# Kernel optimization log

Hardware: AMD Instinct MI355X
Metric: run time of the kernel (lower is better)

Reference implementation:

```python
import jax, jax.numpy as jnp
import numpy as np

B, A, NB = 8, 1024, 64          # batch, atoms, neighbors
NAB, NF, NG, NI = 128, 128, 25, 3  # atom basis, filters, gaussians, interactions
CUT = 5.0
MAXZ = 100
LOG2 = float(np.log(2.0))

def ssp(x):
    # shifted softplus: log(0.5) + softplus(x)
    return jax.nn.softplus(x) - LOG2

def setup_inputs() -> dict:
    key = jax.random.key(0)
    ks = jax.random.split(key, 12)
    positions = jax.random.uniform(ks[0], (B, A, 3), jnp.float32, 0.0, 10.0)
    cell = jnp.zeros((B, 3, 3), jnp.float32)
    cell_offset = jnp.zeros((B, A, NB, 3), jnp.float32)
    # self-avoiding neighbor indices in [0, A)
    off = jax.random.randint(ks[1], (B, A, NB), 1, A)
    neighbors = ((jnp.arange(A)[None, :, None] + off) % A).astype(jnp.int32)
    neighbor_mask = jnp.ones((B, A, NB), jnp.float32)
    atom_mask = jnp.ones((B, A), jnp.float32)
    atomic_numbers = jax.random.randint(ks[2], (B, A), 1, MAXZ).astype(jnp.int32)
    s = 0.05
    emb = (jax.random.normal(ks[3], (MAXZ, NAB)) * 0.1).at[0].set(0.0)  # padding_idx=0
    fw1 = jax.random.normal(ks[4], (NI, NG, NF)) * s
    fb1 = jnp.zeros((NI, NF), jnp.float32)
    fw2 = jax.random.normal(ks[5], (NI, NF, NF)) * s
    fb2 = jnp.zeros((NI, NF), jnp.float32)
    in2f_w = jax.random.normal(ks[6], (NI, NAB, NF)) * s
    f2out_w = jax.random.normal(ks[7], (NI, NF, NAB)) * s
    f2out_b = jnp.zeros((NI, NAB), jnp.float32)
    dense_w = jax.random.normal(ks[8], (NI, NAB, NAB)) * s
    dense_b = jnp.zeros((NI, NAB), jnp.float32)
    return dict(positions=positions, cell=cell, cell_offset=cell_offset,
                neighbor_mask=neighbor_mask, atom_mask=atom_mask,
                emb=emb, fw1=fw1, fb1=fb1, fw2=fw2, fb2=fb2,
                in2f_w=in2f_w, f2out_w=f2out_w, f2out_b=f2out_b,
                dense_w=dense_w, dense_b=dense_b,
                atomic_numbers=atomic_numbers, neighbors=neighbors)

def reference(positions, cell, cell_offset, neighbor_mask, atom_mask,
              emb, fw1, fb1, fw2, fb2, in2f_w, f2out_w, f2out_b,
              dense_w, dense_b, atomic_numbers, neighbors):
    x = emb[atomic_numbers]                                   # (B,A,NAB)
    nb = neighbors.reshape(B, A * NB)
    # atom distances with PBC offsets
    pos_j = jnp.take_along_axis(positions, nb[..., None], axis=1).reshape(B, A, NB, 3)
    pos_j = pos_j + jnp.einsum('banc,bcd->band', cell_offset, cell)
    dvec = pos_j - positions[:, :, None, :]
    d2 = jnp.sum(dvec * dvec, axis=-1)                        # (B,A,NB)
    r_ij = jnp.sqrt(jnp.where(neighbor_mask > 0, d2, 1.0)) * neighbor_mask
    # gaussian smearing of distances
    offsets = jnp.linspace(0.0, CUT, NG, dtype=jnp.float32)
    width = offsets[1] - offsets[0]
    coeff = -0.5 / (width * width)
    f_ij = jnp.exp(coeff * (r_ij[..., None] - offsets) ** 2)  # (B,A,NB,NG)
    # cosine cutoff
    C = 0.5 * (jnp.cos(r_ij * jnp.pi / CUT) + 1.0) * (r_ij < CUT)
    for i in range(NI):
        # filter-generating network
        W = ssp(f_ij @ fw1[i] + fb1[i]) @ fw2[i] + fb2[i]     # (B,A,NB,NF)
        W = W * C[..., None]
        # CFConv: project, gather neighbors, modulate, scatter-sum
        y = x @ in2f_w[i]                                     # (B,A,NF)
        y_nbh = jnp.take_along_axis(y, nb[..., None], axis=1).reshape(B, A, NB, NF)
        agg = jnp.sum(y_nbh * W * neighbor_mask[..., None], axis=2)  # (B,A,NF)
        v = ssp(agg @ f2out_w[i] + f2out_b[i])                # (B,A,NAB)
        v = v @ dense_w[i] + dense_b[i]
        x = x + v
    return x
```

## Files before the change

### kernel.cpp

```cpp
#include <hip/hip_runtime.h>

typedef __attribute__((ext_vector_type(8))) short bf16x8;
typedef __attribute__((ext_vector_type(4))) float f32x4;
typedef __attribute__((ext_vector_type(2))) unsigned int u32x2;
typedef __attribute__((ext_vector_type(4))) unsigned int u32x4;
typedef __attribute__((ext_vector_type(2))) __bf16 bf16x2t;
typedef unsigned short u16;
typedef unsigned int u32;
typedef unsigned long long u64;

#define DI __device__ __forceinline__

#define NKNOT 2048

DI float b2f(u16 u){ union{u32 i; float f;} v; v.i = ((u32)u)<<16; return v.f; }
DI float asf(u32 u){ union{u32 i; float f;} v; v.i = u; return v.f; }
DI u16 f2b(float f){ union{float f; u32 i;} v; v.f=f; u32 u=v.i;
                     return (u16)((u + 0x7fffu + ((u>>16)&1u))>>16); }
DI u32 pk2(float lo, float hi){
#if __has_builtin(__builtin_amdgcn_cvt_pk_bf16_f32)
  bf16x2t h = __builtin_amdgcn_cvt_pk_bf16_f32(lo, hi);
  u32 d; __builtin_memcpy(&d, &h, 4); return d;
#else
  return (u32)f2b(lo) | ((u32)f2b(hi)<<16);
#endif
}
DI float fexp2(float x){
#if __has_builtin(__builtin_amdgcn_exp2f)
  return __builtin_amdgcn_exp2f(x);
#else
  return __expf(x*0.6931471805599453f);
#endif
}
DI float flog2(float x){
#if __has_builtin(__builtin_amdgcn_logf)
  return __builtin_amdgcn_logf(x);
#else
  return __logf(x)*1.4426950408889634f;
#endif
}
DI float ldin(const void* p, size_t i, int isbf){
  return isbf ? b2f(((const u16*)p)[i]) : ((const float*)p)[i];
}
DI f32x4 ldin4(const void* p, size_t i, int isbf){
  if(isbf){
    u32x2 d = *(const u32x2*)((const u16*)p + i);
    f32x4 r;
    r[0] = b2f((u16)(d[0]&0xffff)); r[1] = b2f((u16)(d[0]>>16));
    r[2] = b2f((u16)(d[1]&0xffff)); r[3] = b2f((u16)(d[1]>>16));
    return r;
  }
  return *(const f32x4*)((const float*)p + i);
}
DI int probe_bf(const void* nmask){ return ((const u16*)nmask)[0] == 0x3F80u; }

DI f32x4 mfma16(bf16x8 a, bf16x8 b, f32x4 c){
  return __builtin_amdgcn_mfma_f32_16x16x32_bf16(a,b,c,0,0,0);
}
DI bf16x8 ldfragA_f32(const float* p){
  f32x4 a = ((const f32x4*)p)[0], b = ((const f32x4*)p)[1];
  union{ u32 d[4]; bf16x8 v; } u;
  u.d[0]=pk2(a[0],a[1]); u.d[1]=pk2(a[2],a[3]);
  u.d[2]=pk2(b[0],b[1]); u.d[3]=pk2(b[2],b[3]);
  return u.v;
}
DI float sspf(float x){ return __logf(1.f + __expf(x)) - 0.6931471805599453f; }

#define WF_STRIDE 73728
#define WF_IN2F   24576
#define WF_F2O    40960
#define WF_DEN    57344

__global__ __launch_bounds__(256) void k_setup(const void* __restrict__ pos,
                                               const void* __restrict__ cell,
                                               const void* __restrict__ cello,
                                               const void* __restrict__ nmask,
                                               const void* __restrict__ emb,
                                               const void* __restrict__ fw1,
                                               const void* __restrict__ fb1,
                                               const void* __restrict__ fw2,
                                               const void* __restrict__ fb2,
                                               const void* __restrict__ in2f,
                                               const void* __restrict__ f2o,
                                               const void* __restrict__ den,
                                               const int* __restrict__ z,
                                               const int* __restrict__ nbrs,
                                               float* __restrict__ X,
                                               u32x2* __restrict__ DESC,
                                               u32* __restrict__ CNT,
                                               u16* __restrict__ WF,
                                               u32x2* __restrict__ TT,
                                               float* __restrict__ Y){
  __shared__ __align__(16) u16 Hb[4][16][168];
  int isbf = probe_bf(nmask);
  int bx = blockIdx.x, tid = threadIdx.x;
  int widx = tid>>6;
  int lane = tid & 63;
  int q = lane>>4, l15 = lane&15;

  if(bx < 96){
    int wid = bx*4 + widx;
    int i  = wid>>7;
    int kb = (wid&127)*16;
    u16 (*H)[168] = Hb[widx];

    const float width = 5.0f/24.0f;
    const float c2 = (-0.5f/(width*width))*1.4426950408889634f;
    const float l2e = 1.4426950408889634f;
    float r = (float)(kb + l15) * (5.0f/(float)(NKNOT-1));

    float gv[8];
    #pragma unroll
    for(int j=0;j<8;j++){
      int k = q*8+j;
      if(k < 25){ float t = fmaf(-width,(float)k,r); gv[j] = fexp2(c2*t*t); }
      else gv[j] = (k==25) ? 1.f : 0.f;
    }
    union{ u32 d[4]; bf16x8 v; } afu;
    afu.d[0]=pk2(gv[0],gv[1]); afu.d[1]=pk2(gv[2],gv[3]);
    afu.d[2]=pk2(gv[4],gv[5]); afu.d[3]=pk2(gv[6],gv[7]);
    bf16x8 af = afu.v;

    f32x4 acc[8];
    #pragma unroll
    for(int th=0; th<2; ++th){
      float v[4][8];
      #pragma unroll
      for(int tt=0;tt<4;tt++){
        int c = (th*4+tt)*16 + l15;
        #pragma unroll
        for(int j=0;j<8;j++){
          int k = q*8+j;
          float x;
          if(k < 25)      x = ldin(fw1, (size_t)i*3200 + (size_t)k*128 + c, isbf);
          else if(k==25)  x = ldin(fb1, (size_t)i*128 + c, isbf);
          else            x = 0.f;
          v[tt][j] = x * l2e;
        }
      }
      #pragma unroll
      for(int tt=0;tt<4;tt++){
        union{ u32 d[4]; bf16x8 w; } wu;
        wu.d[0]=pk2(v[tt][0],v[tt][1]); wu.d[1]=pk2(v[tt][2],v[tt][3]);
        wu.d[2]=pk2(v[tt][4],v[tt][5]); wu.d[3]=pk2(v[tt][6],v[tt][7]);
        acc[th*4+tt] = mfma16(wu.w, af, (f32x4){0.f,0.f,0.f,0.f});
      }
    }
    const float ln2 = 0.69314718055994531f;
    #pragma unroll
    for(int t=0;t<8;t++){
      float h0 = fmaf(flog2(1.f+fexp2(acc[t][0])), ln2, -ln2);
      float h1 = fmaf(flog2(1.f+fexp2(acc[t][1])), ln2, -ln2);
      float h2 = fmaf(flog2(1.f+fexp2(acc[t][2])), ln2, -ln2);
      float h3 = fmaf(flog2(1.f+fexp2(acc[t][3])), ln2, -ln2);
      u32x2 d; d[0]=pk2(h0,h1); d[1]=pk2(h2,h3);
      *(u32x2*)(&H[l15][t*16 + q*4]) = d;
    }
    {
      u32x2 zb; zb[0] = (q==0) ? pk2(1.f, 0.f) : 0u; zb[1] = 0u;
      *(u32x2*)(&H[l15][128 + q*4]) = zb;
      u32x2 zz; zz[0]=0u; zz[1]=0u;
      *(u32x2*)(&H[l15][144 + q*4]) = zz;
    }
    #pragma unroll
    for(int t=0;t<8;t++) acc[t] = (f32x4){0.f,0.f,0.f,0.f};
    #pragma unroll
    for(int kk=0;kk<5;kk++){
      bf16x8 a2 = *(const bf16x8*)(&H[l15][kk*32 + q*8]);
      #pragma unroll
      for(int th=0; th<2; ++th){
        float v[4][8];
        #pragma unroll
        for(int tt=0;tt<4;tt++){
          int c = (th*4+tt)*16 + l15;
          #pragma unroll
          for(int j=0;j<8;j++){
            int k = kk*32 + q*8 + j;
            float x;
            if(k < 128)      x = ldin(fw2, (size_t)i*16384 + (size_t)k*128 + c, isbf);
            else if(k==128)  x = ldin(fb2, (size_t)i*128 + c, isbf);
            else             x = 0.f;
            v[tt][j] = x;
          }
        }
        #pragma unroll
        for(int tt=0;tt<4;tt++){
          union{ u32 d[4]; bf16x8 w; } wu;
          wu.d[0]=pk2(v[tt][0],v[tt][1]); wu.d[1]=pk2(v[tt][2],v[tt][3]);
          wu.d[2]=pk2(v[tt][4],v[tt][5]); wu.d[3]=pk2(v[tt][6],v[tt][7]);
          acc[th*4+tt] = mfma16(a2, wu.w, acc[th*4+tt]);
        }
      }
    }
    {
      u32x2* ttb = TT + (size_t)i*NKNOT*64;
      int row = kb + l15;
      #pragma unroll
      for(int t=0;t<8;t++){
        u32 d0 = pk2(acc[t][0],acc[t][1]);
        u32 d1 = pk2(acc[t][2],acc[t][3]);
        int l = t*8 + q*2;
        ((u32*)&ttb[(size_t)row*64 + l    ])[0] = d0;
        ((u32*)&ttb[(size_t)row*64 + l + 1])[0] = d1;
        if(row > 0){
          ((u32*)&ttb[(size_t)(row-1)*64 + l    ])[1] = d0;
          ((u32*)&ttb[(size_t)(row-1)*64 + l + 1])[1] = d1;
        }
      }
    }
    return;
  }
  if(bx < 224){
    int wid2 = (bx-96)*4 + widx;
    int row0 = wid2*16;
    int zr = z[row0 + l15];
    f32x4 acc[8];
    #pragma unroll
    for(int t=0;t<8;t++) acc[t] = (f32x4){0.f,0.f,0.f,0.f};
    #pragma unroll
    for(int kk=0;kk<4;kk++){
      bf16x8 xf;
      if(isbf) xf = *(const bf16x8*)((const u16*)emb + (size_t)zr*128 + kk*32 + q*8);
      else     xf = ldfragA_f32((const float*)emb + (size_t)zr*128 + kk*32 + q*8);
      #pragma unroll
      for(int th=0; th<2; ++th){
        float v[4][8];
        #pragma unroll
        for(int tt=0;tt<4;tt++){
          int c = (th*4+tt)*16 + l15;
          #pragma unroll
          for(int j=0;j<8;j++)
            v[tt][j] = ldin(in2f, (size_t)(kk*32+q*8+j)*128 + c, isbf);
        }
        #pragma unroll
        for(int tt=0;tt<4;tt++){
          union{ u32 d[4]; bf16x8 w; } wu;
          wu.d[0]=pk2(v[tt][0],v[tt][1]); wu.d[1]=pk2(v[tt][2],v[tt][3]);
          wu.d[2]=pk2(v[tt][4],v[tt][5]); wu.d[3]=pk2(v[tt][6],v[tt][7]);
          acc[th*4+tt] = mfma16(wu.w, xf, acc[th*4+tt]);
        }
      }
    }
    #pragma unroll
    for(int t=0;t<8;t++)
      *(f32x4*)(Y + (size_t)(row0+l15)*128 + t*16 + q*4) = acc[t];
    return;
  }
  if(bx < 1248){
    int idx = (bx-224)*256 + tid;
    int a = idx>>5, f4 = (idx&31)*4;
    f32x4 e = ldin4(emb, (size_t)z[a]*128 + f4, isbf);
    *(f32x4*)(X + (size_t)a*128 + f4) = e;
    return;
  }
  if(bx < 3296){
    int pairIdx = (bx-1248)*256 + tid;
    int atom = pairIdx>>6;
    int b = atom>>10;
    int nb = nbrs[pairIdx];
    int jrow = (b<<10) + nb;
    float pi0=ldin(pos,atom*3+0,isbf), pi1=ldin(pos,atom*3+1,isbf), pi2=ldin(pos,atom*3+2,isbf);
    float pj0=ldin(pos,jrow*3+0,isbf), pj1=ldin(pos,jrow*3+1,isbf), pj2=ldin(pos,jrow*3+2,isbf);
    float co0=ldin(cello,(size_t)pairIdx*3+0,isbf),
          co1=ldin(cello,(size_t)pairIdx*3+1,isbf),
          co2=ldin(cello,(size_t)pairIdx*3+2,isbf);
    size_t cb = (size_t)b*9;
    pj0 += co0*ldin(cell,cb+0,isbf) + co1*ldin(cell,cb+3,isbf) + co2*ldin(cell,cb+6,isbf);
    pj1 += co0*ldin(cell,cb+1,isbf) + co1*ldin(cell,cb+4,isbf) + co2*ldin(cell,cb+7,isbf);
    pj2 += co0*ldin(cell,cb+2,isbf) + co1*ldin(cell,cb+5,isbf) + co2*ldin(cell,cb+8,isbf);
    float d0 = pj0-pi0, d1 = pj1-pi1, d2 = pj2-pi2;
    float dd = d0*d0 + d1*d1 + d2*d2;
    float m  = ldin(nmask,pairIdx,isbf);
    float r  = sqrtf(m>0.f ? dd : 1.f) * m;
    float c  = 0.5f*(__cosf(r*3.14159265358979f/5.f)+1.f) * ((r<5.f)?1.f:0.f) * m;
    float s  = r * ((float)(NKNOT-1)/5.0f);
    int   k  = (int)s; if(k > NKNOT-2) k = NKNOT-2;
    float fr = s - (float)k;
    float a0 = c*(1.f-fr), a1 = c*fr;
    union{ _Float16 h[2]; u32 u; } pa;
    pa.h[0] = (_Float16)a0; pa.h[1] = (_Float16)a1;
    int act = (c > 0.f);
    u64 bal = __ballot(act);
    u64 below = bal & ((1ULL<<lane)-1ULL);
    int cnt = (int)__popcll(bal);
    int apre = (int)__popcll(below);
    int pos_ = act ? apre : (cnt + (lane - apre));
    u32x2 dsc;
    if(act){ dsc[0] = pa.u; dsc[1] = (u32)k | ((u32)nb<<16); }
    else   { dsc[0] = 0u;   dsc[1] = 0u; }
    DESC[(size_t)atom*64 + pos_] = dsc;
    if(lane == 0) CNT[atom] = (u32)cnt;
    return;
  }
  {
    int wid = (bx-3296)*4 + widx;
    int i = wid/96, r = wid%96;
    int mat = r>>5, kk = (r>>3)&3, t = r&7;
    const void* src; int off;
    switch(mat){
      case 0:  src = in2f; off=WF_IN2F; break;
      case 1:  src = f2o;  off=WF_F2O;  break;
      default: src = den;  off=WF_DEN;  break;
    }
    size_t sbase = (size_t)i*16384;
    int c = t*16 + l15;
    bf16x8 frag;
    #pragma unroll
    for(int j=0;j<8;j++){
      int k = kk*32 + q*8 + j;
      frag[j] = (short)f2b(ldin(src, sbase + (size_t)k*128 + c, isbf));
    }
    *(bf16x8*)(WF + (size_t)i*WF_STRIDE + off + ((kk*8+t)*64 + lane)*8) = frag;
  }
}

__global__ __launch_bounds__(512, 8) void k_iter(const u32x2* __restrict__ desc,
                                                 const u32* __restrict__ CNT,
                                                 const u32x2* __restrict__ TT,
                                                 const float* __restrict__ Yr,
                                                 float* __restrict__ X,
                                                 float* __restrict__ Yw,
                                                 const u16* __restrict__ f2of,
                                                 const u16* __restrict__ denf,
                                                 const u16* __restrict__ in2fN,
                                                 const void* __restrict__ f2ob,
                                                 const void* __restrict__ denb,
                                                 const void* __restrict__ nmask,
                                                 void* __restrict__ OUT,
                                                 int last, int iidx){
  __shared__ __align__(16) float AGGs[16][132];
  __shared__ __align__(16) u16 Tb[16][136];
  __shared__ __align__(16) u16 Xw[16][136];
  int isbf = probe_bf(nmask);
  int widx = threadIdx.x>>6;
  int lane = threadIdx.x & 63;
  int q = lane>>4, l15 = lane&15;
  int bid = blockIdx.x;
  int row0 = (bid & 7)*1024 + (bid >> 3)*8;

  {
    int atom = row0 + widx;
    int cnt = (int)__builtin_amdgcn_readfirstlane(CNT[atom]);
    int ng  = (cnt + 3) >> 2;
    u32x2 dsc = desc[(size_t)atom*64 + lane];
    const char* Yb = (const char*)(Yr + (size_t)(atom & ~1023)*128);
    const char* Tc = (const char*)TT;
    int h   = lane>>5;
    int j32 = lane&31;
    int boff = j32<<4;
    f32x4 acc4 = (f32x4){0.f,0.f,0.f,0.f};
    #pragma unroll 1
    for(int g=0; g<ng; ++g){
      u32 cu[2]; u32x4 tt[2]; f32x4 yv[2];
      #pragma unroll
      for(int s=0; s<2; ++s){
        int p0 = g*4 + s*2;
        u32 d1a = __builtin_amdgcn_readlane(dsc[1], p0);
        u32 d1b = __builtin_amdgcn_readlane(dsc[1], p0+1);
        u32 d0a = __builtin_amdgcn_readlane(dsc[0], p0);
        u32 d0b = __builtin_amdgcn_readlane(dsc[0], p0+1);
        u32 d1 = h ? d1b : d1a;
        cu[s]  = h ? d0b : d0a;
        u32 krow = d1 & 0xffffu;
        u32 nbr  = d1 >> 16;
        tt[s] = *(const u32x4*)(Tc + ((size_t)krow<<9) + boff);
        yv[s] = *(const f32x4*)(Yb + ((size_t)nbr<<9) + boff);
      }
      #pragma unroll
      for(int s=0; s<2; ++s){
        union{ u32 u; _Float16 hh[2]; } pa; pa.u = cu[s];
        float a0 = (float)pa.hh[0], a1 = (float)pa.hh[1];
        float w0 = fmaf(a1, asf(tt[s][1]<<16),          a0*asf(tt[s][0]<<16));
        float w1 = fmaf(a1, asf(tt[s][1]&0xffff0000u),  a0*asf(tt[s][0]&0xffff0000u));
        float w2 = fmaf(a1, asf(tt[s][3]<<16),          a0*asf(tt[s][2]<<16));
        float w3 = fmaf(a1, asf(tt[s][3]&0xffff0000u),  a0*asf(tt[s][2]&0xffff0000u));
        acc4[0] = fmaf(w0, yv[s][0], acc4[0]);
        acc4[1] = fmaf(w1, yv[s][1], acc4[1]);
        acc4[2] = fmaf(w2, yv[s][2], acc4[2]);
        acc4[3] = fmaf(w3, yv[s][3], acc4[3]);
      }
    }
    *(f32x4*)(&AGGs[widx + 8*h][j32*4]) = acc4;
  }
  __syncthreads();

  {
    int t = widx;
    f32x4 acc = (f32x4){0.f,0.f,0.f,0.f};
    #pragma unroll
    for(int kk=0;kk<4;kk++){
      bf16x8 gf = ldfragA_f32(&AGGs[l15][kk*32 + q*8]);
      bf16x8 wv = *(const bf16x8*)(f2of + ((kk*8+t)*64 + lane)*8);
      acc = mfma16(wv, gf, acc);
    }
    #pragma unroll
    for(int r=0;r<4;r++) acc[r] += __shfl_xor(acc[r], 8);
    f32x4 bv = ldin4(f2ob, (size_t)iidx*128 + t*16 + q*4, isbf);
    u32x2 d;
    d[0] = pk2(sspf(acc[0]+bv[0]), sspf(acc[1]+bv[1]));
    d[1] = pk2(sspf(acc[2]+bv[2]), sspf(acc[3]+bv[3]));
    *(u32x2*)(&Tb[l15][t*16 + q*4]) = d;
  }
  __syncthreads();

  {
    int t = widx;
    f32x4 acc = (f32x4){0.f,0.f,0.f,0.f};
    #pragma unroll
    for(int kk=0;kk<4;kk++){
      bf16x8 tf = *(const bf16x8*)(&Tb[l15][kk*32 + q*8]);
      bf16x8 wv = *(const bf16x8*)(denf + ((kk*8+t)*64 + lane)*8);
      acc = mfma16(wv, tf, acc);
    }
    size_t idx = (size_t)(row0+l15)*128 + t*16 + q*4;
    f32x4 bv = ldin4(denb, (size_t)iidx*128 + t*16 + q*4, isbf);
    f32x4 xv = *(const f32x4*)(X + idx);
    f32x4 xn;
    #pragma unroll
    for(int r=0;r<4;r++) xn[r] = xv[r] + acc[r] + bv[r];
    if(l15 < 8){
      *(f32x4*)(X + idx) = xn;
      if(last){
        if(isbf){
          u32x2 o; o[0]=pk2(xn[0],xn[1]); o[1]=pk2(xn[2],xn[3]);
          *(u32x2*)((u16*)OUT + idx) = o;
        } else {
          *(f32x4*)((float*)OUT + idx) = xn;
        }
      }
    }
    if(!last){
      u32x2 d; d[0]=pk2(xn[0],xn[1]); d[1]=pk2(xn[2],xn[3]);
      *(u32x2*)(&Xw[l15][t*16 + q*4]) = d;
    }
  }
  if(!last){
    __syncthreads();
    {
      int t = widx;
      f32x4 acc = (f32x4){0.f,0.f,0.f,0.f};
      #pragma unroll
      for(int kk=0;kk<4;kk++){
        bf16x8 xf = *(const bf16x8*)(&Xw[l15][kk*32 + q*8]);
        bf16x8 wv = *(const bf16x8*)(in2fN + ((kk*8+t)*64 + lane)*8);
        acc = mfma16(wv, xf, acc);
      }
      if(l15 < 8)
        *(f32x4*)(Yw + (size_t)(row0+l15)*128 + t*16 + q*4) = acc;
    }
  }
}

extern "C" void kernel_launch(void* const* d_in, const int* in_sizes, int n_in,
                              void* d_out, int out_size, void* d_ws, size_t ws_size,
                              hipStream_t stream){
  const void* pos   = d_in[0];
  const void* cell  = d_in[1];
  const void* cello = d_in[2];
  const void* nmask = d_in[3];
  const void* emb   = d_in[5];
  const void* fw1   = d_in[6];
  const void* fb1   = d_in[7];
  const void* fw2   = d_in[8];
  const void* fb2   = d_in[9];
  const void* in2f  = d_in[10];
  const void* f2o   = d_in[11];
  const void* f2ob  = d_in[12];
  const void* den   = d_in[13];
  const void* denb  = d_in[14];
  const int* z      = (const int*)d_in[15];
  const int* nbrs   = (const int*)d_in[16];

  char* ws = (char*)d_ws;
  float* X    = (float*)(ws);
  float* Y    = (float*)(ws +  4194304);
  float* Y2   = (float*)(ws +  8388608);
  u32x2* DESC = (u32x2*)(ws + 12582912);
  u16*   WF   = (u16*)  (ws + 16777216);
  u32x2* TT   = (u32x2*)(ws + 17301504);
  u32*   CNT  = (u32*)  (ws + 20447232);

  k_setup<<<3368, 256, 0, stream>>>(pos, cell, cello, nmask, emb,
                                    fw1, fb1, fw2, fb2, in2f, f2o, den,
                                    z, nbrs, X, DESC, CNT, WF, TT, Y);

  for(int i=0;i<3;i++){
    const u16* base = WF + (size_t)i*WF_STRIDE;
    const u16* in2fN = (i<2) ? (WF + (size_t)(i+1)*WF_STRIDE + WF_IN2F) : WF;
    const float* Yrd = (i&1) ? Y2 : Y;
    float*       Ywr = (i&1) ? Y  : Y2;
    k_iter<<<1024, 512, 0, stream>>>(DESC, CNT, TT + (size_t)i*NKNOT*64, Yrd, X, Ywr,
                                     base + WF_F2O, base + WF_DEN, in2fN,
                                     f2ob, denb, nmask,
                                     d_out, (i==2) ? 1 : 0, i);
  }
}
```

Before: 162.0 us.

## Sort atoms by active-neighbor count to balance per-wave gather loops

Adds a small counting-sort kernel that builds a per-batch permutation of atoms ordered by their count of in-cutoff neighbors. The iteration kernel then assigns each block's eight atoms through this permutation, so waves in a block run similar trip counts in the neighbor gather loop and spend less time idle at the following barrier. In exchange it adds an extra launch, an indirection, and scattered row accesses for X and Y that lose contiguity. It also switches the setup kernel's lane index to tid&63.

```diff
diff --git a/kernel.cpp b/kernel.cpp
--- a/kernel.cpp
+++ b/kernel.cpp
@@ -279,17 +279,18 @@
     float a0 = c*(1.f-fr), a1 = c*fr;
     union{ _Float16 h[2]; u32 u; } pa;
     pa.h[0] = (_Float16)a0; pa.h[1] = (_Float16)a1;
+    int lane2 = tid & 63;
     int act = (c > 0.f);
     u64 bal = __ballot(act);
-    u64 below = bal & ((1ULL<<lane)-1ULL);
+    u64 below = bal & ((1ULL<<lane2)-1ULL);
     int cnt = (int)__popcll(bal);
     int apre = (int)__popcll(below);
-    int pos_ = act ? apre : (cnt + (lane - apre));
+    int pos_ = act ? apre : (cnt + (lane2 - apre));
     u32x2 dsc;
     if(act){ dsc[0] = pa.u; dsc[1] = (u32)k | ((u32)nb<<16); }
     else   { dsc[0] = 0u;   dsc[1] = 0u; }
     DESC[(size_t)atom*64 + pos_] = dsc;
-    if(lane == 0) CNT[atom] = (u32)cnt;
+    if(lane2 == 0) CNT[atom] = (u32)cnt;
     return;
   }
   {
@@ -314,8 +315,32 @@
   }
 }
 
+__global__ __launch_bounds__(256) void k_sort(const u32* __restrict__ CNT,
+                                              int* __restrict__ PERM){
+  __shared__ u32 hist[65];
+  __shared__ u32 pref[65];
+  int b = blockIdx.x;
+  int tid = threadIdx.x;
+  if(tid < 65) hist[tid] = 0;
+  __syncthreads();
+  for(int a = tid; a < 1024; a += 256)
+    atomicAdd(&hist[CNT[b*1024 + a]], 1u);
+  __syncthreads();
+  if(tid == 0){
+    u32 s = 0;
+    for(int i=0;i<65;i++){ pref[i] = s; s += hist[i]; }
+  }
+  __syncthreads();
+  for(int a = tid; a < 1024; a += 256){
+    u32 c = CNT[b*1024 + a];
+    u32 r = atomicAdd(&pref[c], 1u);
+    PERM[b*1024 + r] = b*1024 + a;
+  }
+}
+
 __global__ __launch_bounds__(512, 8) void k_iter(const u32x2* __restrict__ desc,
                                                  const u32* __restrict__ CNT,
+                                                 const int* __restrict__ PERM,
                                                  const u32x2* __restrict__ TT,
                                                  const float* __restrict__ Yr,
                                                  float* __restrict__ X,
@@ -336,10 +361,10 @@
   int lane = threadIdx.x & 63;
   int q = lane>>4, l15 = lane&15;
   int bid = blockIdx.x;
-  int row0 = (bid & 7)*1024 + (bid >> 3)*8;
+  int base = (bid & 7)*1024 + (bid >> 3)*8;
 
   {
-    int atom = row0 + widx;
+    int atom = PERM[base + widx];
     int cnt = (int)__builtin_amdgcn_readfirstlane(CNT[atom]);
     int ng  = (cnt + 3) >> 2;
     u32x2 dsc = desc[(size_t)atom*64 + lane];
@@ -403,6 +428,7 @@
   }
   __syncthreads();
 
+  int arow = PERM[base + (l15 & 7)];
   {
     int t = widx;
     f32x4 acc = (f32x4){0.f,0.f,0.f,0.f};
@@ -412,7 +438,7 @@
       bf16x8 wv = *(const bf16x8*)(denf + ((kk*8+t)*64 + lane)*8);
       acc = mfma16(wv, tf, acc);
     }
-    size_t idx = (size_t)(row0+l15)*128 + t*16 + q*4;
+    size_t idx = (size_t)arow*128 + t*16 + q*4;
     f32x4 bv = ldin4(denb, (size_t)iidx*128 + t*16 + q*4, isbf);
     f32x4 xv = *(const f32x4*)(X + idx);
     f32x4 xn;
@@ -446,7 +472,7 @@
         acc = mfma16(wv, xf, acc);
       }
       if(l15 < 8)
-        *(f32x4*)(Yw + (size_t)(row0+l15)*128 + t*16 + q*4) = acc;
+        *(f32x4*)(Yw + (size_t)arow*128 + t*16 + q*4) = acc;
     }
   }
 }
@@ -479,17 +505,20 @@
   u16*   WF   = (u16*)  (ws + 16777216);
   u32x2* TT   = (u32x2*)(ws + 17301504);
   u32*   CNT  = (u32*)  (ws + 20447232);
+  int*   PERM = (int*)  (ws + 20480000);
 
   k_setup<<<3368, 256, 0, stream>>>(pos, cell, cello, nmask, emb,
                                     fw1, fb1, fw2, fb2, in2f, f2o, den,
                                     z, nbrs, X, DESC, CNT, WF, TT, Y);
+  k_sort <<<   8, 256, 0, stream>>>(CNT, PERM);
 
   for(int i=0;i<3;i++){
     const u16* base = WF + (size_t)i*WF_STRIDE;
     const u16* in2fN = (i<2) ? (WF + (size_t)(i+1)*WF_STRIDE + WF_IN2F) : WF;
     const float* Yrd = (i&1) ? Y2 : Y;
     float*       Ywr = (i&1) ? Y  : Y2;
-    k_iter<<<1024, 512, 0, stream>>>(DESC, CNT, TT + (size_t)i*NKNOT*64, Yrd, X, Ywr,
+    k_iter<<<1024, 512, 0, stream>>>(DESC, CNT, PERM, TT + (size_t)i*NKNOT*64,
+                                     Yrd, X, Ywr,
                                      base + WF_F2O, base + WF_DEN, in2fN,
                                      f2ob, denb, nmask,
                                      d_out, (i==2) ? 1 : 0, i);
```

Measured after the change: 167.1 us. +3.2%, slower.
